# Kernel optimization log

Measured on AMD Instinct MI355X. Metric: run time of the kernel, lower is better.

Reference implementation:

```python
import math
import jax, jax.numpy as jnp
import numpy as np

SDE_THRESHOLD = 10.0
ANGLE_THRESHOLD_DEG = 30.0


def setup_inputs() -> dict:
    key = jax.random.key(0)
    k1, k2 = jax.random.split(key)
    B, H, N = 8, 16, 1024
    y_pred = jax.random.normal(k1, (B, H, 4), dtype=jnp.float32)
    sample_points = jax.random.normal(k2, (B, N, 3), dtype=jnp.float32)
    return {"y_pred": y_pred, "sample_points": sample_points}


def reference(y_pred, sample_points):
    # y_pred: [B,H,4] = (nx,ny,nz,d) per plane head; sample_points: [B,N,3]
    B, H, _ = y_pred.shape
    n = y_pred[..., :3]
    n = n / jnp.linalg.norm(n, axis=-1, keepdims=True)  # normalize normals
    d = y_pred[..., 3]

    # transform_representation_cm: represent plane by (normal, point) where
    # point = projection of the point-cloud centroid onto the plane n.x + d = 0
    cm = sample_points.mean(axis=1)  # [B,3]
    point = cm[:, None, :] - (jnp.einsum('bhd,bd->bh', n, cm) + d)[..., None] * n  # [B,H,3]

    # chamfer_adapter: reflect points across each plane, bidirectional chamfer (squared dists)
    proj = jnp.einsum('bnd,bhd->bhn', sample_points, n) + d[:, :, None]  # [B,H,N]
    refl = sample_points[:, None, :, :] - 2.0 * proj[..., None] * n[:, :, None, :]  # [B,H,N,3]
    rr = jnp.sum(refl * refl, axis=-1)                  # [B,H,N]
    ss = jnp.sum(sample_points * sample_points, axis=-1)  # [B,N]
    cross = jnp.einsum('bhid,bjd->bhij', refl, sample_points)  # [B,H,N,N]
    d2 = rr[..., None] + ss[:, None, None, :] - 2.0 * cross
    sde = jnp.min(d2, axis=-1).mean(axis=-1) + jnp.min(d2, axis=-2).mean(axis=-1)  # [B,H]

    # minmax_normalization -> confidence = 1 - (sde - min) / |max - min| per batch row
    mn = sde.min(axis=1, keepdims=True)
    mx = sde.max(axis=1, keepdims=True)
    conf = 1.0 - (sde - mn) / jnp.abs(mx - mn)

    # pairwise angle-based duplicate suppression (vectorized NMS)
    cos = jnp.clip(jnp.einsum('bhd,bgd->bhg', n, n), -1.0, 1.0)
    ang = jnp.arccos(cos) * (180.0 / math.pi)
    close = (ang < ANGLE_THRESHOLD_DEG) | (180.0 - ang < ANGLE_THRESHOLD_DEG)
    close = close & ~jnp.eye(H, dtype=bool)
    valid = sde <= SDE_THRESHOLD  # filter x.sde <= sde_threshold
    # plane i is popped iff exists valid j (close) with sde_i >= sde_j (equal sde pops both)
    sup = valid & jnp.any(close & valid[:, None, :] & (sde[:, :, None] >= sde[:, None, :]), axis=-1)
    keep = valid & ~sup

    # to_tensor(): [normal(3), point(3), confidence, sde]; sort kept by confidence desc,
    # zero-pad suppressed/filtered slots (fixed shape [B,H,8] instead of ragged pad_sequence)
    planes = jnp.concatenate([n, point, conf[..., None], sde[..., None]], axis=-1)  # [B,H,8]
    sort_key = jnp.where(keep, conf, -jnp.inf)
    order = jnp.argsort(-sort_key, axis=1)
    planes_s = jnp.take_along_axis(planes, order[..., None], axis=1)
    keep_s = jnp.take_along_axis(keep, order, axis=1)
    return jnp.where(keep_s[..., None], planes_s, 0.0)
```

## Files before the change

kernel.cpp:

```cpp
#include <hip/hip_runtime.h>
#include <math.h>

#define BB 8
#define HH 16
#define NN 1024
#define TB 256
#define POWN 2
#define OCH 512
#define SCH 512


__global__ __launch_bounds__(TB) void chamfer_kernel(
    const float* __restrict__ y_pred,
    const float* __restrict__ sp,
    float* __restrict__ ws)
{
    __shared__ __align__(16) float4 pts[SCH];

    const int blk = blockIdx.x;
    const int bh  = blk >> 2;
    const int oh  = (blk >> 1) & 1;
    const int sh  = blk & 1;
    const int b   = bh >> 4;
    const int tid = threadIdx.x;

    float pnx = y_pred[bh * 4 + 0];
    float pny = y_pred[bh * 4 + 1];
    float pnz = y_pred[bh * 4 + 2];
    float pd  = y_pred[bh * 4 + 3];
    float inv = 1.0f / sqrtf(pnx * pnx + pny * pny + pnz * pnz);
    pnx *= inv; pny *= inv; pnz *= inv;

    const float* spb = sp + (size_t)b * NN * 3;

    for (int k = tid; k < SCH; k += TB) {
        int j = sh * SCH + k;
        float x = spb[j * 3 + 0], y = spb[j * 3 + 1], z = spb[j * 3 + 2];
        pts[k] = make_float4(x, y, z, x * x + y * y + z * z);
    }

    float mx[POWN], my[POWN], mz[POWN], osq[POWN];
#pragma unroll
    for (int u = 0; u < POWN; ++u) {
        int i = oh * OCH + u * TB + tid;
        float x = spb[i * 3 + 0], y = spb[i * 3 + 1], z = spb[i * 3 + 2];
        float proj = x * pnx + y * pny + z * pnz + pd;
        x -= 2.0f * proj * pnx;
        y -= 2.0f * proj * pny;
        z -= 2.0f * proj * pnz;
        osq[u] = x * x + y * y + z * z;
        mx[u] = -2.0f * x; my[u] = -2.0f * y; mz[u] = -2.0f * z;
    }
    __syncthreads();

    float m0[POWN], m1[POWN], m2[POWN], m3[POWN];
#pragma unroll
    for (int u = 0; u < POWN; ++u) { m0[u] = 3.4e38f; m1[u] = 3.4e38f; m2[u] = 3.4e38f; m3[u] = 3.4e38f; }

    for (int j = 0; j < SCH; j += 4) {
        float4 qa = pts[j + 0];
        float4 qb = pts[j + 1];
        float4 qc = pts[j + 2];
        float4 qd = pts[j + 3];
#pragma unroll
        for (int u = 0; u < POWN; ++u) {
            m0[u] = fminf(m0[u], fmaf(mx[u], qa.x, fmaf(my[u], qa.y, fmaf(mz[u], qa.z, qa.w))));
            m1[u] = fminf(m1[u], fmaf(mx[u], qb.x, fmaf(my[u], qb.y, fmaf(mz[u], qb.z, qb.w))));
            m2[u] = fminf(m2[u], fmaf(mx[u], qc.x, fmaf(my[u], qc.y, fmaf(mz[u], qc.z, qc.w))));
            m3[u] = fminf(m3[u], fmaf(mx[u], qd.x, fmaf(my[u], qd.y, fmaf(mz[u], qd.z, qd.w))));
        }
    }

    float* wp = ws + ((size_t)(bh * 2 + sh)) * NN + oh * OCH;
#pragma unroll
    for (int u = 0; u < POWN; ++u)
        wp[u * TB + tid] = osq[u] + fminf(fminf(m0[u], m1[u]), fminf(m2[u], m3[u]));
}

__global__ __launch_bounds__(TB) void finalize_kernel(
    const float* __restrict__ ws,
    const float* __restrict__ y_pred,
    const float* __restrict__ sp,
    float* __restrict__ out)
{
    const int b   = blockIdx.x;
    const int tid = threadIdx.x;

    __shared__ float sde_s[HH], nx_s[HH], ny_s[HH], nz_s[HH], d_s[HH], conf_s[HH];
    __shared__ float cmacc[3];
    __shared__ int keep_s[HH];

    if (tid < HH) sde_s[tid] = 0.0f;
    if (tid < 3)  cmacc[tid] = 0.0f;
    __syncthreads();

    const float* spb = sp + (size_t)b * NN * 3;
    float sx = 0.0f, sy = 0.0f, sz = 0.0f;
    for (int p = tid; p < NN; p += TB) {
        sx += spb[p * 3 + 0];
        sy += spb[p * 3 + 1];
        sz += spb[p * 3 + 2];
    }
    for (int off = 32; off; off >>= 1) {
        sx += __shfl_down(sx, off, 64);
        sy += __shfl_down(sy, off, 64);
        sz += __shfl_down(sz, off, 64);
    }
    if ((tid & 63) == 0) {
        atomicAdd(&cmacc[0], sx);
        atomicAdd(&cmacc[1], sy);
        atomicAdd(&cmacc[2], sz);
    }

    {
        const int h   = tid >> 4;
        const int sub = tid & 15;
        const float* p0 = ws + ((size_t)((b * HH + h) * 2 + 0)) * NN;
        const float* p1 = ws + ((size_t)((b * HH + h) * 2 + 1)) * NN;
        float acc = 0.0f;
        for (int k = 0; k < 64; ++k) {
            int i = sub * 64 + k;
            acc += fminf(p0[i], p1[i]);
        }
        atomicAdd(&sde_s[h], acc);
    }
    __syncthreads();

    const float cmx = cmacc[0] / NN, cmy = cmacc[1] / NN, cmz = cmacc[2] / NN;

    if (tid < HH) {
        int h = tid;
        float nx = y_pred[(b * HH + h) * 4 + 0];
        float ny = y_pred[(b * HH + h) * 4 + 1];
        float nz = y_pred[(b * HH + h) * 4 + 2];
        float d  = y_pred[(b * HH + h) * 4 + 3];
        float inv = 1.0f / sqrtf(nx * nx + ny * ny + nz * nz);
        nx *= inv; ny *= inv; nz *= inv;
        nx_s[h] = nx; ny_s[h] = ny; nz_s[h] = nz; d_s[h] = d;
        sde_s[h] = sde_s[h] * (2.0f / NN);
    }
    __syncthreads();

    if (tid < HH) {
        int h = tid;
        float mn = sde_s[0], mx = sde_s[0];
        for (int g = 1; g < HH; ++g) {
            mn = fminf(mn, sde_s[g]);
            mx = fmaxf(mx, sde_s[g]);
        }
        float sde  = sde_s[h];
        float conf = 1.0f - (sde - mn) / fabsf(mx - mn);
        conf_s[h]  = conf;
        bool valid = (sde <= 10.0f);
        bool sup   = false;
        if (valid) {
            for (int g = 0; g < HH; ++g) {
                if (g == h) continue;
                float c = nx_s[h] * nx_s[g] + ny_s[h] * ny_s[g] + nz_s[h] * nz_s[g];
                c = fminf(1.0f, fmaxf(-1.0f, c));
                float ang = acosf(c) * 57.29577951308232f;
                bool close = (ang < 30.0f) || (180.0f - ang < 30.0f);
                if (close && (sde_s[g] <= 10.0f) && (sde >= sde_s[g])) sup = true;
            }
        }
        keep_s[h] = (valid && !sup) ? 1 : 0;
    }
    __syncthreads();

    if (tid < HH) {
        int h = tid;
        float keyh = keep_s[h] ? conf_s[h] : -INFINITY;
        int pos = 0;
        for (int g = 0; g < HH; ++g) {
            float keyg = keep_s[g] ? conf_s[g] : -INFINITY;
            if (keyg > keyh || (keyg == keyh && g < h)) ++pos;
        }
        float nx = nx_s[h], ny = ny_s[h], nz = nz_s[h];
        float t  = nx * cmx + ny * cmy + nz * cmz + d_s[h];
        float px = cmx - t * nx, py = cmy - t * ny, pz = cmz - t * nz;

        float* o = out + (size_t)(b * HH + pos) * 8;
        if (keep_s[h]) {
            o[0] = nx; o[1] = ny; o[2] = nz;
            o[3] = px; o[4] = py; o[5] = pz;
            o[6] = conf_s[h];
            o[7] = sde_s[h];
        } else {
            for (int c = 0; c < 8; ++c) o[c] = 0.0f;
        }
    }
}

extern "C" void kernel_launch(void* const* d_in, const int* in_sizes, int n_in,
                              void* d_out, int out_size, void* d_ws, size_t ws_size,
                              hipStream_t stream) {
    const float* y_pred = (const float*)d_in[0];
    const float* sp     = (const float*)d_in[1];
    float* out          = (float*)d_out;
    float* ws           = (float*)d_ws;

    chamfer_kernel<<<dim3(BB * HH * 4), dim3(TB), 0, stream>>>(y_pred, sp, ws);
    finalize_kernel<<<dim3(BB), dim3(TB), 0, stream>>>(ws, y_pred, sp, out);
}
```

Baseline: 76.77 us.

## Split chamfer work by source chunks only, with more owned points per thread

The chamfer grid now splits each batch-head only across four source-point chunks of 256, and every thread owns four reflected points. Each float4 read from LDS is therefore reused across more distance evaluations. The inner loop prefetches the next four LDS points into registers and keeps only two min accumulators per owned point. The finalize kernel now reduces four partial-min arrays per head using float4 loads, which doubles the workspace traffic and adds register pressure in exchange for less LDS traffic.

Measured after the change: 83.18 us. +8.4%, slower.

```diff
diff --git a/kernel.cpp b/kernel.cpp
--- a/kernel.cpp
+++ b/kernel.cpp
@@ -5,9 +5,9 @@
 #define HH 16
 #define NN 1024
 #define TB 256
-#define POWN 2
-#define OCH 512
-#define SCH 512
+#define POWN 4
+#define NSC 4
+#define SCH 256
 
 
 __global__ __launch_bounds__(TB) void chamfer_kernel(
@@ -19,8 +19,7 @@
 
     const int blk = blockIdx.x;
     const int bh  = blk >> 2;
-    const int oh  = (blk >> 1) & 1;
-    const int sh  = blk & 1;
+    const int sc  = blk & (NSC - 1);
     const int b   = bh >> 4;
     const int tid = threadIdx.x;
 
@@ -33,16 +32,16 @@
 
     const float* spb = sp + (size_t)b * NN * 3;
 
-    for (int k = tid; k < SCH; k += TB) {
-        int j = sh * SCH + k;
+    {
+        int j = sc * SCH + tid;
         float x = spb[j * 3 + 0], y = spb[j * 3 + 1], z = spb[j * 3 + 2];
-        pts[k] = make_float4(x, y, z, x * x + y * y + z * z);
+        pts[tid] = make_float4(x, y, z, x * x + y * y + z * z);
     }
 
     float mx[POWN], my[POWN], mz[POWN], osq[POWN];
 #pragma unroll
     for (int u = 0; u < POWN; ++u) {
-        int i = oh * OCH + u * TB + tid;
+        int i = u * TB + tid;
         float x = spb[i * 3 + 0], y = spb[i * 3 + 1], z = spb[i * 3 + 2];
         float proj = x * pnx + y * pny + z * pnz + pd;
         x -= 2.0f * proj * pnx;
@@ -53,28 +52,40 @@
     }
     __syncthreads();
 
-    float m0[POWN], m1[POWN], m2[POWN], m3[POWN];
+    float m0[POWN], m1[POWN];
 #pragma unroll
-    for (int u = 0; u < POWN; ++u) { m0[u] = 3.4e38f; m1[u] = 3.4e38f; m2[u] = 3.4e38f; m3[u] = 3.4e38f; }
-
-    for (int j = 0; j < SCH; j += 4) {
-        float4 qa = pts[j + 0];
-        float4 qb = pts[j + 1];
-        float4 qc = pts[j + 2];
-        float4 qd = pts[j + 3];
-#pragma unroll
-        for (int u = 0; u < POWN; ++u) {
-            m0[u] = fminf(m0[u], fmaf(mx[u], qa.x, fmaf(my[u], qa.y, fmaf(mz[u], qa.z, qa.w))));
-            m1[u] = fminf(m1[u], fmaf(mx[u], qb.x, fmaf(my[u], qb.y, fmaf(mz[u], qb.z, qb.w))));
-            m2[u] = fminf(m2[u], fmaf(mx[u], qc.x, fmaf(my[u], qc.y, fmaf(mz[u], qc.z, qc.w))));
-            m3[u] = fminf(m3[u], fmaf(mx[u], qd.x, fmaf(my[u], qd.y, fmaf(mz[u], qd.z, qd.w))));
-        }
-    }
-
-    float* wp = ws + ((size_t)(bh * 2 + sh)) * NN + oh * OCH;
+    for (int u = 0; u < POWN; ++u) { m0[u] = 3.4e38f; m1[u] = 3.4e38f; }
+
+#define DIST(q, u) fmaf(mx[u], q.x, fmaf(my[u], q.y, fmaf(mz[u], q.z, q.w)))
+#define STEP4 do { \
+    _Pragma("unroll") \
+    for (int u = 0; u < POWN; ++u) { \
+        float da = DIST(qa, u); \
+        float db = DIST(qb, u); \
+        float dc = DIST(qc, u); \
+        float dd = DIST(qd, u); \
+        m0[u] = fminf(fminf(m0[u], da), db); \
+        m1[u] = fminf(fminf(m1[u], dc), dd); \
+    } } while (0)
+
+    float4 qa = pts[0], qb = pts[1], qc = pts[2], qd = pts[3];
+    for (int j = 0; j < SCH - 4; j += 4) {
+        float4 na = pts[j + 4];
+        float4 nb = pts[j + 5];
+        float4 nc = pts[j + 6];
+        float4 nd = pts[j + 7];
+        STEP4;
+        qa = na; qb = nb; qc = nc; qd = nd;
+    }
+    STEP4;
+
+#undef STEP4
+#undef DIST
+
+    float* wp = ws + (size_t)(bh * NSC + sc) * NN;
 #pragma unroll
     for (int u = 0; u < POWN; ++u)
-        wp[u * TB + tid] = osq[u] + fminf(fminf(m0[u], m1[u]), fminf(m2[u], m3[u]));
+        wp[u * TB + tid] = osq[u] + fminf(m0[u], m1[u]);
 }
 
 __global__ __launch_bounds__(TB) void finalize_kernel(
@@ -115,12 +126,20 @@
     {
         const int h   = tid >> 4;
         const int sub = tid & 15;
-        const float* p0 = ws + ((size_t)((b * HH + h) * 2 + 0)) * NN;
-        const float* p1 = ws + ((size_t)((b * HH + h) * 2 + 1)) * NN;
+        const float* base = ws + (size_t)((b * HH + h) * NSC) * NN;
+        const float4* q0 = (const float4*)(base);
+        const float4* q1 = (const float4*)(base + NN);
+        const float4* q2 = (const float4*)(base + 2 * NN);
+        const float4* q3 = (const float4*)(base + 3 * NN);
         float acc = 0.0f;
-        for (int k = 0; k < 64; ++k) {
-            int i = sub * 64 + k;
-            acc += fminf(p0[i], p1[i]);
+        for (int g = 0; g < 16; ++g) {
+            int i4 = sub * 16 + g;
+            float4 a0 = q0[i4], a1 = q1[i4], a2 = q2[i4], a3 = q3[i4];
+            float e0 = fminf(fminf(a0.x, a1.x), fminf(a2.x, a3.x));
+            float e1 = fminf(fminf(a0.y, a1.y), fminf(a2.y, a3.y));
+            float e2 = fminf(fminf(a0.z, a1.z), fminf(a2.z, a3.z));
+            float e3 = fminf(fminf(a0.w, a1.w), fminf(a2.w, a3.w));
+            acc += (e0 + e1) + (e2 + e3);
         }
         atomicAdd(&sde_s[h], acc);
     }
@@ -199,6 +218,6 @@
     float* out          = (float*)d_out;
     float* ws           = (float*)d_ws;
 
-    chamfer_kernel<<<dim3(BB * HH * 4), dim3(TB), 0, stream>>>(y_pred, sp, ws);
+    chamfer_kernel<<<dim3(BB * HH * NSC), dim3(TB), 0, stream>>>(y_pred, sp, ws);
     finalize_kernel<<<dim3(BB), dim3(TB), 0, stream>>>(ws, y_pred, sp, out);
 }
```
